# Kernel tuning notes

Measured on AMD Instinct MI355X. Metric: run time of the kernel, lower is better.

## Reference

```python
import jax, jax.numpy as jnp
import numpy as np

N = 50000      # amino-acid nodes
DIN = 64       # input feature dim
DH = 64        # hidden dim (= GAT out_feats per head)
H = 4          # attention heads
E_RES, E_SEQ, E_KNN = 400000, 100000, 400000
EPS = 1e-5


def setup_inputs() -> dict:
    key = jax.random.key(0)
    ks = iter(jax.random.split(key, 32))
    def nrm(shape, scale=0.1):
        return jax.random.normal(next(ks), shape, dtype=jnp.float32) * scale
    def edges(E):
        s = jax.random.randint(next(ks), (E,), 0, N, dtype=jnp.int32)
        d = jax.random.randint(next(ks), (E,), 0, N, dtype=jnp.int32)
        return s, d
    x = nrm((N, DIN), 1.0)
    src_res, dst_res = edges(E_RES)
    src_seq, dst_seq = edges(E_SEQ)
    src_knn, dst_knn = edges(E_KNN)
    inp = dict(x=x, src_res=src_res, dst_res=dst_res, src_seq=src_seq,
               dst_seq=dst_seq, src_knn=src_knn, dst_knn=dst_knn)
    # layer 0 (in=DIN), layer 1 (in=DH): per-relation stacked GAT params
    inp.update(W0=nrm((3, DIN, H * DH)), al0=nrm((3, H, DH)), ar0=nrm((3, H, DH)),
               b0=nrm((3, H * DH)), rW0=nrm((3, DIN, H * DH)))
    inp.update(W1=nrm((3, DH, H * DH)), al1=nrm((3, H, DH)), ar1=nrm((3, H, DH)),
               b1=nrm((3, H * DH)), rW1=nrm((3, DH, H * DH)))
    inp.update(fcW0=nrm((DH, DH)), fcb0=nrm((DH,)), fcW1=nrm((DH, DH)), fcb1=nrm((DH,)))
    inp.update(g0=jnp.ones((DIN,), jnp.float32), be0=jnp.zeros((DIN,), jnp.float32),
               g1=jnp.ones((DH,), jnp.float32), be1=jnp.zeros((DH,), jnp.float32))
    return inp


def _bn(x, g, b):
    mu = jnp.mean(x, axis=0)
    var = jnp.mean((x - mu) ** 2, axis=0)
    return (x - mu) * jax.lax.rsqrt(var + EPS) * g + b


def _gat(h, src, dst, W, al, ar, bias, rW):
    # DGL GATConv (feat_drop off in eval, residual=True via res_fc Linear, bias)
    n = h.shape[0]
    fs = (h @ W).reshape(n, H, DH)                    # [N,H,D]
    el = jnp.sum(fs * al, axis=-1)                    # [N,H]
    er = jnp.sum(fs * ar, axis=-1)
    e = jax.nn.leaky_relu(el[src] + er[dst], 0.2)     # [E,H]
    m = jax.ops.segment_max(e, dst, num_segments=n)
    a = jnp.exp(e - m[dst])
    s = jax.ops.segment_sum(a, dst, num_segments=n)
    alpha = a / s[dst]                                # edge-softmax per dst/head
    rst = jax.ops.segment_sum(alpha[:, :, None] * fs[src], dst, num_segments=n)
    return rst + (h @ rW).reshape(n, H, DH) + bias.reshape(1, H, DH)


def _layer(x, edges, W, al, ar, b, rW, fcW, fcb, g, be):
    x = _bn(x, g, be)
    h = jnp.zeros((x.shape[0], H, DH), x.dtype)
    for r, (s_, d_) in enumerate(edges):              # 3 relation types, summed
        h = h + _gat(x, s_, d_, W[r], al[r], ar[r], b[r], rW[r])
    x = jnp.mean(h, axis=1)                           # mean over heads
    return jax.nn.relu(x @ fcW + fcb)


def reference(x, src_res, dst_res, src_seq, dst_seq, src_knn, dst_knn,
              W0, al0, ar0, b0, rW0, W1, al1, ar1, b1, rW1,
              fcW0, fcb0, fcW1, fcb1, g0, be0, g1, be1):
    edges = [(src_res, dst_res), (src_seq, dst_seq), (src_knn, dst_knn)]
    x = _layer(x, edges, W0, al0, ar0, b0, rW0, fcW0, fcb0, g0, be0)
    x = _layer(x, edges, W1, al1, ar1, b1, rW1, fcW1, fcb1, g1, be1)
    return x
```

## Files before the change

kernel.cpp:

```cpp
#include <hip/hip_runtime.h>
#include <math.h>

#define NN    50000
#define DD    64
#define HH    4
#define E_RES 400000
#define E_SEQ 100000
#define E_KNN 400000
#define ETOT  (E_RES+E_SEQ+E_KNN)
#define RPS   (NN + 4)
#define NBLK  ((NN+255)/256)
#define KTOT  864
#define CTPS  (ETOT + 32)
#define NBUK  98
#define TBUK  (3*NBUK)
#define EPB   4096
#define PABLK ((ETOT+EPB-1)/EPB)
#define FBLK  (NN/16)
#define LZS   808

typedef __attribute__((ext_vector_type(8))) short short8;
typedef __attribute__((ext_vector_type(4))) float floatx4;

__device__ inline unsigned short f2bf(float f){
  union{float f; unsigned u;} v; v.f=f;
  unsigned r = v.u + 0x7FFF + ((v.u>>16)&1);
  return (unsigned short)(r>>16);
}
__device__ inline float bf2f(unsigned short u){
  union{unsigned u; float f;} v; v.u=(unsigned)u<<16; return v.f;
}

__global__ void __launch_bounds__(256)
k_bucketcnt(const int* __restrict__ d0, const int* __restrict__ d1,
            const int* __restrict__ d2, int* __restrict__ bcnt){
  __shared__ int cnt[TBUK];
  int t = threadIdx.x;
  for(int i=t;i<TBUK;i+=256) cnt[i]=0;
  __syncthreads();
  int ebase = blockIdx.x*EPB;
  #pragma unroll
  for(int j=0;j<16;j++){
    int i = ebase + j*256 + t;
    int d, r;
    if(i < E_RES){ d=d0[i]; r=0; }
    else if(i < E_RES+E_SEQ){ d=d1[i-E_RES]; r=1; }
    else if(i < ETOT){ d=d2[i-E_RES-E_SEQ]; r=2; }
    else continue;
    atomicAdd(&cnt[r*NBUK + (d>>9)], 1);
  }
  __syncthreads();
  for(int i=t;i<TBUK;i+=256){ int c=cnt[i]; if(c) atomicAdd(&bcnt[i], c); }
}

__global__ void k_bucketscan(const int* __restrict__ bcnt,
                             int* __restrict__ bbase, int* __restrict__ bcur){
  __shared__ int sh[TBUK];
  int t = threadIdx.x;
  if(t < 64){
    int carry = 0;
    for(int c=0;c<5;c++){
      int idx = c*64 + t;
      int v = (idx < TBUK) ? bcnt[idx] : 0;
      int inc = v;
      for(int off=1; off<64; off<<=1){ int n=__shfl_up(inc, off, 64); if(t>=off) inc+=n; }
      if(idx < TBUK) sh[idx] = carry + inc - v;
      carry += __shfl(inc, 63, 64);
    }
  }
  __syncthreads();
  if(t < TBUK){ bbase[t] = sh[t]; bcur[t] = sh[t]; }
  if(t == 0) bbase[TBUK] = ETOT;
}

__global__ void __launch_bounds__(256)
k_partA(const int* __restrict__ s0, const int* __restrict__ d0,
        const int* __restrict__ s1, const int* __restrict__ d1,
        const int* __restrict__ s2, const int* __restrict__ d2,
        int* __restrict__ bcur, unsigned* __restrict__ pairs){
  __shared__ int cnt[TBUK];
  __shared__ int gb[TBUK];
  int t = threadIdx.x;
  for(int i=t;i<TBUK;i+=256) cnt[i]=0;
  __syncthreads();
  int ebase = blockIdx.x*EPB;
  unsigned meta[16], pk[16];
  #pragma unroll
  for(int j=0;j<16;j++){
    int i = ebase + j*256 + t;
    int s, d, r;
    if(i < E_RES){ s=s0[i]; d=d0[i]; r=0; }
    else if(i < E_RES+E_SEQ){ int k=i-E_RES; s=s1[k]; d=d1[k]; r=1; }
    else if(i < ETOT){ int k=i-E_RES-E_SEQ; s=s2[k]; d=d2[k]; r=2; }
    else { meta[j]=0xFFFFFFFFu; continue; }
    int bk = r*NBUK + (d>>9);
    int rk = atomicAdd(&cnt[bk], 1);
    meta[j] = ((unsigned)bk<<16) | (unsigned)rk;
    pk[j]   = ((unsigned)(d&511)<<16) | (unsigned)s;
  }
  __syncthreads();
  for(int i=t;i<TBUK;i+=256){ int c=cnt[i]; gb[i] = c ? atomicAdd(&bcur[i], c) : 0; }
  __syncthreads();
  #pragma unroll
  for(int j=0;j<16;j++){
    unsigned mt = meta[j];
    if(mt != 0xFFFFFFFFu)
      pairs[gb[mt>>16] + (mt & 0xFFFFu)] = pk[j];
  }
}

__global__ void __launch_bounds__(256)
k_partB(const unsigned* __restrict__ pairs, const int* __restrict__ bbase,
        int* __restrict__ rowptr, int* __restrict__ csr){
  int bb = blockIdx.x, r = bb / NBUK, b = bb - r*NBUK;
  int dbase = b*512, dmax = min(512, NN - dbase);
  int off = (r==0)?0:(r==1)?E_RES:(E_RES+E_SEQ);
  __shared__ int hist[512];
  __shared__ int curs[513];
  int t = threadIdx.x;
  hist[t]=0; hist[256+t]=0;
  __syncthreads();
  int beg = bbase[bb], end = bbase[bb+1];
  for(int i=beg+t; i<end; i+=256) atomicAdd(&hist[pairs[i]>>16], 1);
  __syncthreads();
  if(t < 64){
    int carry = 0;
    for(int c=0;c<8;c++){
      int v = hist[c*64+t];
      int inc = v;
      for(int o2=1; o2<64; o2<<=1){ int n=__shfl_up(inc, o2, 64); if(t>=o2) inc+=n; }
      curs[c*64+t] = (beg - off) + carry + inc - v;
      carry += __shfl(inc, 63, 64);
    }
    if(t==0) curs[512] = end - off;
  }
  __syncthreads();
  int* rp = rowptr + r*RPS + dbase;
  for(int i=t; i<=dmax; i+=256) rp[i] = curs[i];
  __syncthreads();
  for(int i=beg+t; i<end; i+=256){
    unsigned p = pairs[i];
    int pos = atomicAdd(&curs[p>>16], 1);
    csr[off + pos] = (int)(p & 0xFFFFu);
  }
}

__global__ void k_bnstats(const float* __restrict__ x, float* __restrict__ stats,
                          unsigned short* __restrict__ Abf){
  __shared__ float sh[512];
  int t = threadIdx.x, col = t & 63, rg = t >> 6;
  float s=0.f, q=0.f;
  for(int row = blockIdx.x*4 + rg; row < NN; row += gridDim.x*4){
    float v = x[(size_t)row*64 + col]; s += v; q += v*v;
    Abf[(size_t)row*64 + col] = f2bf(v);
  }
  sh[t]=s; sh[256+t]=q; __syncthreads();
  if(rg==0){
    s = sh[col]+sh[64+col]+sh[128+col]+sh[192+col];
    q = sh[256+col]+sh[320+col]+sh[384+col]+sh[448+col];
    atomicAdd(&stats[col], s); atomicAdd(&stats[64+col], q);
  }
}

__global__ void __launch_bounds__(256)
k_prep3(const float* __restrict__ stats, const float* __restrict__ g,
        const float* __restrict__ be, const float* __restrict__ W,
        const float* __restrict__ al, const float* __restrict__ ar,
        const float* __restrict__ b, const float* __restrict__ rW,
        const float* __restrict__ fcW, const float* __restrict__ fcb,
        float* __restrict__ wbufF){
  __shared__ float scale[64], shift[64];
  int t = threadIdx.x;
  if(t<64){
    float mu  = stats[t]*(1.0f/NN);
    float var = stats[64+t]*(1.0f/NN) - mu*mu;
    float sc  = g[t]*rsqrtf(var + 1e-5f);
    scale[t]=sc; shift[t]=be[t]-mu*sc;
  }
  __syncthreads();
  char* wb = (char*)wbufF;
  unsigned short* Wf = (unsigned short*)wbufF;
  float* biasF = (float*)(wb + 110592);
  int bid = blockIdx.x;
  if(bid < 52){
    __shared__ float fcWs[4096];
    for(int i=t;i<4096;i+=256) fcWs[i]=fcW[i];
    __syncthreads();
    int j = bid*16 + (t>>4);
    int cg = (t&15)*4;
    float Wrow[64];
    if(j < 64){
      for(int d=0; d<64; d++){
        float w=0.f;
        for(int r=0;r<3;r++)
          #pragma unroll
          for(int h=0;h<4;h++)
            w += rW[((size_t)(r*64+j))*256 + h*64 + d];
        Wrow[d] = scale[j]*0.25f*w;
      }
    } else {
      int jj = j-64;
      int r = jj>>8, dc = jj&255, h = dc&3, c = dc>>2;
      const float* Wp = W + ((size_t)(r*64+c))*256 + h*64;
      float sc = 0.25f*scale[c];
      #pragma unroll
      for(int d=0; d<64; d++) Wrow[d] = sc*Wp[d];
    }
    #pragma unroll
    for(int cc=0; cc<4; cc++){
      int col = cg+cc;
      float acc=0.f;
      #pragma unroll
      for(int d=0; d<64; d++) acc += Wrow[d]*fcWs[d*64+col];
      Wf[(size_t)col*KTOT + j] = f2bf(acc);
    }
  } else if(bid < 58){
    int wv = (bid-52)*4 + (t>>6);
    int r = wv >> 3, cc = wv & 7, h = cc & 3, k = t & 63;
    const float* av = ((cc>=4)?ar:al) + (r*HH+h)*64;
    const float* Wk = W + ((size_t)(r*64+k))*256 + h*64;
    float w=0.f;
    for(int d2=0; d2<64; d2++) w += Wk[d2]*av[d2];
    float* WelR = (float*)(wb + 110848 + r*2080);
    WelR[cc*64 + k] = scale[k]*w;
    float bp = shift[k]*w;
    for(int off=32; off; off>>=1) bp += __shfl_down(bp, off, 64);
    if(k==0) (WelR + 512)[cc] = bp;
  } else {
    __shared__ float S[3][64];
    __shared__ float BH[64];
    if(t<192){
      int r=t>>6, d=t&63;
      float s=0.f;
      #pragma unroll
      for(int h=0;h<4;h++){
        const float* Wp = W + (size_t)(r*64)*256 + h*64 + d;
        for(int k=0;k<64;k++) s += shift[k]*Wp[(size_t)k*256];
      }
      S[r][d]=0.25f*s;
    } else {
      int d = t-192;
      float s=0.f;
      for(int k=0;k<64;k++){
        float w=0.f;
        for(int r=0;r<3;r++)
          #pragma unroll
          for(int h=0;h<4;h++)
            w += rW[((size_t)(r*64+k))*256 + h*64 + d];
        s += shift[k]*0.25f*w;
      }
      float bb=0.f;
      for(int r=0;r<3;r++)
        #pragma unroll
        for(int h=0;h<4;h++) bb += b[r*256 + h*64 + d];
      BH[d] = s + 0.25f*bb;
    }
    __syncthreads();
    if(t<192){
      int r=t>>6, col=t&63;
      float acc=0.f;
      for(int d=0;d<64;d++) acc += S[r][d]*fcW[d*64+col];
      Wf[(size_t)col*KTOT + 832 + r] = f2bf(acc);
    } else {
      int col=t-192;
      float acc=0.f;
      for(int d=0;d<64;d++) acc += BH[d]*fcW[d*64+col];
      biasF[col] = acc + fcb[col];
    }
    if(t<64){
      for(int j=835;j<KTOT;j++) Wf[(size_t)t*KTOT + j] = 0;
    }
  }
}

__global__ void __launch_bounds__(256)
k_el3(const float* __restrict__ A, const float* __restrict__ wbufF,
      float* __restrict__ EL){
  int r = blockIdx.x / NBLK;
  const char* wb = (const char*)wbufF;
  const float* Wel = (const float*)(wb + 110848 + r*2080);
  const float* biasE = Wel + 512;
  float* ELr = EL + (size_t)r*NN*8;
  __shared__ float sw[512];
  __shared__ float sb[8];
  int t = threadIdx.x;
  sw[t]=Wel[t]; sw[256+t]=Wel[256+t];
  if(t<8) sb[t]=biasE[t];
  __syncthreads();
  int n = (blockIdx.x % NBLK)*256 + t;
  if(n>=NN) return;
  float acc[8];
  #pragma unroll
  for(int c=0;c<8;c++) acc[c]=sb[c];
  const float4* Ar = (const float4*)(A + (size_t)n*64);
  #pragma unroll
  for(int kq=0;kq<16;kq++){
    float4 a = Ar[kq];
    #pragma unroll
    for(int c=0;c<8;c++){
      const float* w = sw + c*64 + kq*4;
      acc[c] += a.x*w[0] + a.y*w[1] + a.z*w[2] + a.w*w[3];
    }
  }
  ((float4*)ELr)[n*2]   = make_float4(acc[0],acc[1],acc[2],acc[3]);
  ((float4*)ELr)[n*2+1] = make_float4(acc[4],acc[5],acc[6],acc[7]);
}

__global__ void __launch_bounds__(256)
k_edgecoef3(const float* __restrict__ EL, const int* __restrict__ rowptr,
            const int* __restrict__ csr, unsigned short* __restrict__ coefT){
  int r = blockIdx.x / NBLK;
  const float* ELr = EL + (size_t)r*NN*8;
  const int* rp = rowptr + r*RPS;
  int off = (r==0)?0:(r==1)?E_RES:(E_RES+E_SEQ);
  const int* cs = csr + off;
  unsigned short* t0 = coefT + off;
  unsigned short* t1 = coefT + (size_t)CTPS + off;
  unsigned short* t2 = coefT + (size_t)2*CTPS + off;
  unsigned short* t3 = coefT + (size_t)3*CTPS + off;
  int n = (blockIdx.x % NBLK)*256 + threadIdx.x;
  if(n>=NN) return;
  int beg = rp[n], end = rp[n+1];
  if(end<=beg) return;
  const float4 er = ((const float4*)ELr)[n*2+1];
  float m0=-1e30f,m1=-1e30f,m2=-1e30f,m3=-1e30f;
  float s0=0.f,s1=0.f,s2=0.f,s3=0.f;
  for(int i=beg;i<end;i++){
    int src = cs[i];
    float4 el = ((const float4*)ELr)[src*2];
    float e0=el.x+er.x, e1=el.y+er.y, e2=el.z+er.z, e3=el.w+er.w;
    e0 = e0>0.f? e0 : 0.2f*e0;
    e1 = e1>0.f? e1 : 0.2f*e1;
    e2 = e2>0.f? e2 : 0.2f*e2;
    e3 = e3>0.f? e3 : 0.2f*e3;
    float n0=fmaxf(m0,e0); s0=s0*__expf(m0-n0)+__expf(e0-n0); m0=n0;
    float n1=fmaxf(m1,e1); s1=s1*__expf(m1-n1)+__expf(e1-n1); m1=n1;
    float n2=fmaxf(m2,e2); s2=s2*__expf(m2-n2)+__expf(e2-n2); m2=n2;
    float n3=fmaxf(m3,e3); s3=s3*__expf(m3-n3)+__expf(e3-n3); m3=n3;
  }
  float r0=1.f/s0, r1=1.f/s1, r2=1.f/s2, r3=1.f/s3;
  for(int i=beg;i<end;i++){
    int src = cs[i];
    float4 el = ((const float4*)ELr)[src*2];
    float e0=el.x+er.x, e1=el.y+er.y, e2=el.z+er.z, e3=el.w+er.w;
    e0 = e0>0.f? e0 : 0.2f*e0;
    e1 = e1>0.f? e1 : 0.2f*e1;
    e2 = e2>0.f? e2 : 0.2f*e2;
    e3 = e3>0.f? e3 : 0.2f*e3;
    t0[i] = f2bf(__expf(e0-m0)*r0);
    t1[i] = f2bf(__expf(e1-m1)*r1);
    t2[i] = f2bf(__expf(e2-m2)*r2);
    t3[i] = f2bf(__expf(e3-m3)*r3);
  }
}

__global__ void __launch_bounds__(256)
k_fused(const unsigned short* __restrict__ Abf, const int* __restrict__ rowptr,
        const int* __restrict__ csr, const unsigned short* __restrict__ coefT,
        const float* __restrict__ wbufF, float* __restrict__ out,
        unsigned short* __restrict__ Abf2, float* __restrict__ stats, int dostats){
  __shared__ unsigned short Zl[16*LZS];
  const unsigned short* Wf = (const unsigned short*)wbufF;
  const float* biasF = (const float*)((const char*)wbufF + 110592);
  int t = threadIdx.x, wv = t>>6, lane = t&63, m = lane&15, kq = lane>>4;
  int nb = blockIdx.x*16;
  int n4 = nb + wv*4;
  int nn = m>>2, h = m&3;
  for(int i=t; i<512; i+=256){ int nd=i>>5, j=i&31; if(j<29) Zl[nd*LZS+771+j]=0; }
  for(int r=0;r<3;r++){
    const int* rp = rowptr + r*RPS;
    int off = (r==0)?0:(r==1)?E_RES:(E_RES+E_SEQ);
    const int* cs = csr + off;
    const unsigned short* cT = coefT + (size_t)h*CTPS + off;
    int rpn  = rp[n4+nn];
    int rpn1 = rp[n4+nn+1];
    unsigned dg = (unsigned)(rpn1 - rpn);
    int beg = __shfl(rpn, 0, 64);
    int end = __shfl(rpn1, 15, 64);
    floatx4 acc0={0.f,0.f,0.f,0.f};
    floatx4 acc1={0.f,0.f,0.f,0.f};
    floatx4 acc2={0.f,0.f,0.f,0.f};
    floatx4 acc3={0.f,0.f,0.f,0.f};
    for(int eb = (beg & ~31); eb < end; eb += 32){
      int p0 = eb + kq*8;
      union { uint4 q; short8 v; } af;
      af.q = *(const uint4*)(cT + p0);
      int qd = p0 - rpn;
      unsigned w0 = (((unsigned)(qd+0)<dg)?0x0000FFFFu:0u) | (((unsigned)(qd+1)<dg)?0xFFFF0000u:0u);
      unsigned w1 = (((unsigned)(qd+2)<dg)?0x0000FFFFu:0u) | (((unsigned)(qd+3)<dg)?0xFFFF0000u:0u);
      unsigned w2 = (((unsigned)(qd+4)<dg)?0x0000FFFFu:0u) | (((unsigned)(qd+5)<dg)?0xFFFF0000u:0u);
      unsigned w3 = (((unsigned)(qd+6)<dg)?0x0000FFFFu:0u) | (((unsigned)(qd+7)<dg)?0xFFFF0000u:0u);
      af.q.x &= w0; af.q.y &= w1; af.q.z &= w2; af.q.w &= w3;
      const int* csp = cs + p0;
      int s0=csp[0],s1=csp[1],s2=csp[2],s3=csp[3],s4=csp[4],s5=csp[5],s6=csp[6],s7=csp[7];
      const unsigned short* q0 = Abf + ((size_t)s0<<6) + m;
      const unsigned short* q1 = Abf + ((size_t)s1<<6) + m;
      const unsigned short* q2 = Abf + ((size_t)s2<<6) + m;
      const unsigned short* q3 = Abf + ((size_t)s3<<6) + m;
      const unsigned short* q4 = Abf + ((size_t)s4<<6) + m;
      const unsigned short* q5 = Abf + ((size_t)s5<<6) + m;
      const unsigned short* q6 = Abf + ((size_t)s6<<6) + m;
      const unsigned short* q7 = Abf + ((size_t)s7<<6) + m;
      union { unsigned u[4]; short8 v; } b0,b1,b2,b3;
      b0.u[0]=(unsigned)q0[0] |((unsigned)q1[0]<<16);
      b0.u[1]=(unsigned)q2[0] |((unsigned)q3[0]<<16);
      b0.u[2]=(unsigned)q4[0] |((unsigned)q5[0]<<16);
      b0.u[3]=(unsigned)q6[0] |((unsigned)q7[0]<<16);
      b1.u[0]=(unsigned)q0[16]|((unsigned)q1[16]<<16);
      b1.u[1]=(unsigned)q2[16]|((unsigned)q3[16]<<16);
      b1.u[2]=(unsigned)q4[16]|((unsigned)q5[16]<<16);
      b1.u[3]=(unsigned)q6[16]|((unsigned)q7[16]<<16);
      b2.u[0]=(unsigned)q0[32]|((unsigned)q1[32]<<16);
      b2.u[1]=(unsigned)q2[32]|((unsigned)q3[32]<<16);
      b2.u[2]=(unsigned)q4[32]|((unsigned)q5[32]<<16);
      b2.u[3]=(unsigned)q6[32]|((unsigned)q7[32]<<16);
      b3.u[0]=(unsigned)q0[48]|((unsigned)q1[48]<<16);
      b3.u[1]=(unsigned)q2[48]|((unsigned)q3[48]<<16);
      b3.u[2]=(unsigned)q4[48]|((unsigned)q5[48]<<16);
      b3.u[3]=(unsigned)q6[48]|((unsigned)q7[48]<<16);
      acc0 = __builtin_amdgcn_mfma_f32_16x16x32_bf16(af.v, b0.v, acc0, 0,0,0);
      acc1 = __builtin_amdgcn_mfma_f32_16x16x32_bf16(af.v, b1.v, acc1, 0,0,0);
      acc2 = __builtin_amdgcn_mfma_f32_16x16x32_bf16(af.v, b2.v, acc2, 0,0,0);
      acc3 = __builtin_amdgcn_mfma_f32_16x16x32_bf16(af.v, b3.v, acc3, 0,0,0);
    }
    unsigned short* zrow = Zl + (wv*4+kq)*LZS + r*256 + m*4;
    ushort4 o;
    o.x=f2bf(acc0[0]); o.y=f2bf(acc0[1]); o.z=f2bf(acc0[2]); o.w=f2bf(acc0[3]);
    *(ushort4*)(zrow)       = o;
    o.x=f2bf(acc1[0]); o.y=f2bf(acc1[1]); o.z=f2bf(acc1[2]); o.w=f2bf(acc1[3]);
    *(ushort4*)(zrow + 64)  = o;
    o.x=f2bf(acc2[0]); o.y=f2bf(acc2[1]); o.z=f2bf(acc2[2]); o.w=f2bf(acc2[3]);
    *(ushort4*)(zrow + 128) = o;
    o.x=f2bf(acc3[0]); o.y=f2bf(acc3[1]); o.z=f2bf(acc3[2]); o.w=f2bf(acc3[3]);
    *(ushort4*)(zrow + 192) = o;
    int degk = __shfl((int)dg, kq<<2, 64);
    if(m==0)
      Zl[(wv*4+kq)*LZS + 768 + r] = degk>0 ? (unsigned short)0x3F80 : (unsigned short)0;
  }
  __syncthreads();
  floatx4 acc = {0.f,0.f,0.f,0.f};
  const unsigned short* Arow = Abf + (size_t)(nb+m)*64;
  const unsigned short* Zrow = Zl + m*LZS;
  #pragma unroll
  for(int kb=0; kb<27; kb++){
    short8 a;
    if(kb<2) a = *(const short8*)(Arow + kb*32 + kq*8);
    else     a = *(const short8*)(Zrow + (kb-2)*32 + kq*8);
    short8 b = *(const short8*)(Wf + (size_t)(wv*16+m)*KTOT + kb*32 + kq*8);
    acc = __builtin_amdgcn_mfma_f32_16x16x32_bf16(a, b, acc, 0,0,0);
  }
  int col = wv*16 + m;
  float bb = biasF[col];
  float sv=0.f, qv=0.f;
  #pragma unroll
  for(int ri=0; ri<4; ri++){
    int ro = nb + kq*4 + ri;
    float v = fmaxf(acc[ri] + bb, 0.f);
    out[(size_t)ro*64 + col] = v;
    if(dostats){
      Abf2[(size_t)ro*64 + col] = f2bf(v);
      sv += v; qv += v*v;
    }
  }
  if(dostats){
    sv += __shfl_xor(sv, 16, 64); qv += __shfl_xor(qv, 16, 64);
    sv += __shfl_xor(sv, 32, 64); qv += __shfl_xor(qv, 32, 64);
    if(kq==0){ atomicAdd(&stats[col], sv); atomicAdd(&stats[64+col], qv); }
  }
}

extern "C" void kernel_launch(void* const* d_in, const int* in_sizes, int n_in,
                              void* d_out, int out_size, void* d_ws, size_t ws_size,
                              hipStream_t stream){
  const float* x      =(const float*)d_in[0];
  const int* src_res  =(const int*)d_in[1];
  const int* dst_res  =(const int*)d_in[2];
  const int* src_seq  =(const int*)d_in[3];
  const int* dst_seq  =(const int*)d_in[4];
  const int* src_knn  =(const int*)d_in[5];
  const int* dst_knn  =(const int*)d_in[6];
  const float* W0 =(const float*)d_in[7];
  const float* al0=(const float*)d_in[8];
  const float* ar0=(const float*)d_in[9];
  const float* b0 =(const float*)d_in[10];
  const float* rW0=(const float*)d_in[11];
  const float* W1 =(const float*)d_in[12];
  const float* al1=(const float*)d_in[13];
  const float* ar1=(const float*)d_in[14];
  const float* b1 =(const float*)d_in[15];
  const float* rW1=(const float*)d_in[16];
  const float* fcW0=(const float*)d_in[17];
  const float* fcb0=(const float*)d_in[18];
  const float* fcW1=(const float*)d_in[19];
  const float* fcb1=(const float*)d_in[20];
  const float* g0 =(const float*)d_in[21];
  const float* be0=(const float*)d_in[22];
  const float* g1 =(const float*)d_in[23];
  const float* be1=(const float*)d_in[24];

  char* ws=(char*)d_ws;
  int*   bcnt   =(int*)  (ws+0);
  int*   bbase  =(int*)  (ws+4096);
  float* stats0 =(float*)(ws+600000);
  float* stats1 =(float*)(ws+600512);
  int*   rowptr =(int*)  (ws+601024);
  int*   bcur   =(int*)  (ws+1201088);
  int*   csr    =(int*)  (ws+1801088);
  float* wbuf   =(float*)(ws+5401088);
  unsigned short* Abf  =(unsigned short*)(ws+5526528);
  unsigned* pairs =(unsigned*)(ws+11926528UL);
  float* xbuf   =(float*)(ws+91926528UL);
  float* EL     =(float*)(ws+104726528UL);
  unsigned short* coefT=(unsigned short*)(ws+109526528UL);
  unsigned short* Abf2 =(unsigned short*)(ws+123926528UL);

  hipMemsetAsync(ws, 0, 601024, stream);

  k_bucketcnt<<<PABLK,256,0,stream>>>(dst_res,dst_seq,dst_knn,bcnt);
  k_bucketscan<<<1,512,0,stream>>>(bcnt,bbase,bcur);
  k_partA<<<PABLK,256,0,stream>>>(src_res,dst_res,src_seq,dst_seq,
                                  src_knn,dst_knn,bcur,pairs);
  k_partB<<<TBUK,256,0,stream>>>(pairs,bbase,rowptr,csr);

  k_bnstats<<<256,256,0,stream>>>(x,stats0,Abf);
  k_prep3<<<59,256,0,stream>>>(stats0,g0,be0,W0,al0,ar0,b0,rW0,fcW0,fcb0,wbuf);
  k_el3<<<3*NBLK,256,0,stream>>>(x,wbuf,EL);
  k_edgecoef3<<<3*NBLK,256,0,stream>>>(EL,rowptr,csr,coefT);
  k_fused<<<FBLK,256,0,stream>>>(Abf,rowptr,csr,coefT,wbuf,xbuf,Abf2,stats1,1);
  k_prep3<<<59,256,0,stream>>>(stats1,g1,be1,W1,al1,ar1,b1,rW1,fcW1,fcb1,wbuf);
  k_el3<<<3*NBLK,256,0,stream>>>(xbuf,wbuf,EL);
  k_edgecoef3<<<3*NBLK,256,0,stream>>>(EL,rowptr,csr,coefT);
  k_fused<<<FBLK,256,0,stream>>>(Abf2,rowptr,csr,coefT,wbuf,(float*)d_out,Abf2,stats0,0);
}
```

Measured before the change: 430.5 us.

## Split fused GAT kernel across relations with 12 waves and split-K epilogue

The fused aggregation kernel now launches 768 threads per block, giving each relation its own group of four waves instead of looping over the three relations serially inside one wave. The final 27-step MFMA projection is split three ways along K across the wave groups, and the partial sums are reduced through a new shared-memory buffer before bias, ReLU and stats. The Z row stride grows slightly and the zero-fill loop is rewritten to cover the padding. This is meant to raise parallelism and latency hiding in the gather-heavy edge loop. In exchange it adds an extra barrier, more shared memory per block, and possible register-pressure limits at 768 threads.

```diff
diff --git a/kernel.cpp b/kernel.cpp
--- a/kernel.cpp
+++ b/kernel.cpp
@@ -17,7 +17,7 @@
 #define EPB   4096
 #define PABLK ((ETOT+EPB-1)/EPB)
 #define FBLK  (NN/16)
-#define LZS   808
+#define LZS   810
 
 typedef __attribute__((ext_vector_type(8))) short short8;
 typedef __attribute__((ext_vector_type(4))) float floatx4;
@@ -354,20 +354,22 @@
   }
 }
 
-__global__ void __launch_bounds__(256)
+__global__ void __launch_bounds__(768)
 k_fused(const unsigned short* __restrict__ Abf, const int* __restrict__ rowptr,
         const int* __restrict__ csr, const unsigned short* __restrict__ coefT,
         const float* __restrict__ wbufF, float* __restrict__ out,
         unsigned short* __restrict__ Abf2, float* __restrict__ stats, int dostats){
   __shared__ unsigned short Zl[16*LZS];
+  __shared__ float pf[8*256];
   const unsigned short* Wf = (const unsigned short*)wbufF;
   const float* biasF = (const float*)((const char*)wbufF + 110592);
   int t = threadIdx.x, wv = t>>6, lane = t&63, m = lane&15, kq = lane>>4;
   int nb = blockIdx.x*16;
-  int n4 = nb + wv*4;
+  int sg = wv & 3, r = wv >> 2;
+  int n4 = nb + sg*4;
   int nn = m>>2, h = m&3;
-  for(int i=t; i<512; i+=256){ int nd=i>>5, j=i&31; if(j<29) Zl[nd*LZS+771+j]=0; }
-  for(int r=0;r<3;r++){
+  for(int i=t; i<624; i+=768){ int nd=i/39, j=i-nd*39; Zl[nd*LZS+771+j]=0; }
+  {
     const int* rp = rowptr + r*RPS;
     int off = (r==0)?0:(r==1)?E_RES:(E_RES+E_SEQ);
     const int* cs = csr + off;
@@ -423,7 +425,7 @@
       acc2 = __builtin_amdgcn_mfma_f32_16x16x32_bf16(af.v, b2.v, acc2, 0,0,0);
       acc3 = __builtin_amdgcn_mfma_f32_16x16x32_bf16(af.v, b3.v, acc3, 0,0,0);
     }
-    unsigned short* zrow = Zl + (wv*4+kq)*LZS + r*256 + m*4;
+    unsigned short* zrow = Zl + (sg*4+kq)*LZS + r*256 + m*4;
     ushort4 o;
     o.x=f2bf(acc0[0]); o.y=f2bf(acc0[1]); o.z=f2bf(acc0[2]); o.w=f2bf(acc0[3]);
     *(ushort4*)(zrow)       = o;
@@ -435,37 +437,49 @@
     *(ushort4*)(zrow + 192) = o;
     int degk = __shfl((int)dg, kq<<2, 64);
     if(m==0)
-      Zl[(wv*4+kq)*LZS + 768 + r] = degk>0 ? (unsigned short)0x3F80 : (unsigned short)0;
-  }
-  __syncthreads();
+      Zl[(sg*4+kq)*LZS + 768 + r] = degk>0 ? (unsigned short)0x3F80 : (unsigned short)0;
+  }
+  __syncthreads();
+  int ct = wv & 3, ks = wv >> 2;
   floatx4 acc = {0.f,0.f,0.f,0.f};
   const unsigned short* Arow = Abf + (size_t)(nb+m)*64;
   const unsigned short* Zrow = Zl + m*LZS;
   #pragma unroll
-  for(int kb=0; kb<27; kb++){
+  for(int kk=0; kk<9; kk++){
+    int kb = ks*9 + kk;
     short8 a;
     if(kb<2) a = *(const short8*)(Arow + kb*32 + kq*8);
     else     a = *(const short8*)(Zrow + (kb-2)*32 + kq*8);
-    short8 b = *(const short8*)(Wf + (size_t)(wv*16+m)*KTOT + kb*32 + kq*8);
+    short8 b = *(const short8*)(Wf + (size_t)(ct*16+m)*KTOT + kb*32 + kq*8);
     acc = __builtin_amdgcn_mfma_f32_16x16x32_bf16(a, b, acc, 0,0,0);
   }
-  int col = wv*16 + m;
-  float bb = biasF[col];
-  float sv=0.f, qv=0.f;
-  #pragma unroll
-  for(int ri=0; ri<4; ri++){
-    int ro = nb + kq*4 + ri;
-    float v = fmaxf(acc[ri] + bb, 0.f);
-    out[(size_t)ro*64 + col] = v;
+  if(ks != 0)
+    ((float4*)pf)[(wv-4)*64 + lane] = make_float4(acc[0],acc[1],acc[2],acc[3]);
+  __syncthreads();
+  if(ks == 0){
+    float4 p1 = ((float4*)pf)[(ct  )*64 + lane];
+    float4 p2 = ((float4*)pf)[(ct+4)*64 + lane];
+    int col = ct*16 + m;
+    float bb = biasF[col];
+    float vr0 = acc[0]+p1.x+p2.x, vr1 = acc[1]+p1.y+p2.y;
+    float vr2 = acc[2]+p1.z+p2.z, vr3 = acc[3]+p1.w+p2.w;
+    float sv=0.f, qv=0.f;
+    float vv[4] = {vr0,vr1,vr2,vr3};
+    #pragma unroll
+    for(int ri=0; ri<4; ri++){
+      int ro = nb + kq*4 + ri;
+      float v = fmaxf(vv[ri] + bb, 0.f);
+      out[(size_t)ro*64 + col] = v;
+      if(dostats){
+        Abf2[(size_t)ro*64 + col] = f2bf(v);
+        sv += v; qv += v*v;
+      }
+    }
     if(dostats){
-      Abf2[(size_t)ro*64 + col] = f2bf(v);
-      sv += v; qv += v*v;
-    }
-  }
-  if(dostats){
-    sv += __shfl_xor(sv, 16, 64); qv += __shfl_xor(qv, 16, 64);
-    sv += __shfl_xor(sv, 32, 64); qv += __shfl_xor(qv, 32, 64);
-    if(kq==0){ atomicAdd(&stats[col], sv); atomicAdd(&stats[64+col], qv); }
+      sv += __shfl_xor(sv, 16, 64); qv += __shfl_xor(qv, 16, 64);
+      sv += __shfl_xor(sv, 32, 64); qv += __shfl_xor(qv, 32, 64);
+      if(kq==0){ atomicAdd(&stats[col], sv); atomicAdd(&stats[64+col], qv); }
+    }
   }
 }
 
@@ -526,9 +540,9 @@
   k_prep3<<<59,256,0,stream>>>(stats0,g0,be0,W0,al0,ar0,b0,rW0,fcW0,fcb0,wbuf);
   k_el3<<<3*NBLK,256,0,stream>>>(x,wbuf,EL);
   k_edgecoef3<<<3*NBLK,256,0,stream>>>(EL,rowptr,csr,coefT);
-  k_fused<<<FBLK,256,0,stream>>>(Abf,rowptr,csr,coefT,wbuf,xbuf,Abf2,stats1,1);
+  k_fused<<<FBLK,768,0,stream>>>(Abf,rowptr,csr,coefT,wbuf,xbuf,Abf2,stats1,1);
   k_prep3<<<59,256,0,stream>>>(stats1,g1,be1,W1,al1,ar1,b1,rW1,fcW1,fcb1,wbuf);
   k_el3<<<3*NBLK,256,0,stream>>>(xbuf,wbuf,EL);
   k_edgecoef3<<<3*NBLK,256,0,stream>>>(EL,rowptr,csr,coefT);
-  k_fused<<<FBLK,256,0,stream>>>(Abf2,rowptr,csr,coefT,wbuf,(float*)d_out,Abf2,stats0,0);
-}
+  k_fused<<<FBLK,768,0,stream>>>(Abf2,rowptr,csr,coefT,wbuf,(float*)d_out,Abf2,stats0,0);
+}
```

Measured after the change: 468.6 us. +8.9%, slower.

## Stage gathered source rows through LDS with vector loads in fused GAT kernel

Applied to the files above, without the earlier changes.

The edge-aggregation loop used to build each MFMA B-fragment from sixteen scattered 2-byte global loads per lane. It now has each lane pair fetch one full 128-byte source row with four 16-byte loads and store it into a per-wave LDS staging tile (padded stride). B-fragments are then read from LDS. Explicit lgkmcnt waits and sched barriers order the LDS writes and reads within each wave. The Zl stride is also tweaked and the pairs workspace buffer is relocated. The trade-off is extra LDS traffic, LDS capacity and synchronisation stalls in exchange for coalesced global access.

```diff
diff --git a/kernel.cpp b/kernel.cpp
--- a/kernel.cpp
+++ b/kernel.cpp
@@ -17,7 +17,8 @@
 #define EPB   4096
 #define PABLK ((ETOT+EPB-1)/EPB)
 #define FBLK  (NN/16)
-#define LZS   808
+#define LZS   810
+#define SGS   72
 
 typedef __attribute__((ext_vector_type(8))) short short8;
 typedef __attribute__((ext_vector_type(4))) float floatx4;
@@ -360,12 +361,16 @@
         const float* __restrict__ wbufF, float* __restrict__ out,
         unsigned short* __restrict__ Abf2, float* __restrict__ stats, int dostats){
   __shared__ unsigned short Zl[16*LZS];
+  __shared__ unsigned short Sg[4*32*SGS];
   const unsigned short* Wf = (const unsigned short*)wbufF;
   const float* biasF = (const float*)((const char*)wbufF + 110592);
   int t = threadIdx.x, wv = t>>6, lane = t&63, m = lane&15, kq = lane>>4;
   int nb = blockIdx.x*16;
   int n4 = nb + wv*4;
   int nn = m>>2, h = m&3;
+  int srow = lane>>1, shalf = lane&1;
+  unsigned short* sgw = Sg + (wv*32 + srow)*SGS + shalf*32;
+  const unsigned short* sgr = Sg + (size_t)(wv*32 + kq*8)*SGS;
   for(int i=t; i<512; i+=256){ int nd=i>>5, j=i&31; if(j<29) Zl[nd*LZS+771+j]=0; }
   for(int r=0;r<3;r++){
     const int* rp = rowptr + r*RPS;
@@ -391,37 +396,34 @@
       unsigned w2 = (((unsigned)(qd+4)<dg)?0x0000FFFFu:0u) | (((unsigned)(qd+5)<dg)?0xFFFF0000u:0u);
       unsigned w3 = (((unsigned)(qd+6)<dg)?0x0000FFFFu:0u) | (((unsigned)(qd+7)<dg)?0xFFFF0000u:0u);
       af.q.x &= w0; af.q.y &= w1; af.q.z &= w2; af.q.w &= w3;
-      const int* csp = cs + p0;
-      int s0=csp[0],s1=csp[1],s2=csp[2],s3=csp[3],s4=csp[4],s5=csp[5],s6=csp[6],s7=csp[7];
-      const unsigned short* q0 = Abf + ((size_t)s0<<6) + m;
-      const unsigned short* q1 = Abf + ((size_t)s1<<6) + m;
-      const unsigned short* q2 = Abf + ((size_t)s2<<6) + m;
-      const unsigned short* q3 = Abf + ((size_t)s3<<6) + m;
-      const unsigned short* q4 = Abf + ((size_t)s4<<6) + m;
-      const unsigned short* q5 = Abf + ((size_t)s5<<6) + m;
-      const unsigned short* q6 = Abf + ((size_t)s6<<6) + m;
-      const unsigned short* q7 = Abf + ((size_t)s7<<6) + m;
+      int srcr = cs[eb + srow];
+      const unsigned short* rowp = Abf + ((size_t)srcr<<6) + shalf*32;
+      uint4 g0 = *(const uint4*)(rowp);
+      uint4 g1 = *(const uint4*)(rowp + 8);
+      uint4 g2 = *(const uint4*)(rowp + 16);
+      uint4 g3 = *(const uint4*)(rowp + 24);
+      *(uint4*)(sgw)      = g0;
+      *(uint4*)(sgw + 8)  = g1;
+      *(uint4*)(sgw + 16) = g2;
+      *(uint4*)(sgw + 24) = g3;
+      asm volatile("s_waitcnt lgkmcnt(0)" ::: "memory");
+      __builtin_amdgcn_sched_barrier(0);
       union { unsigned u[4]; short8 v; } b0,b1,b2,b3;
-      b0.u[0]=(unsigned)q0[0] |((unsigned)q1[0]<<16);
-      b0.u[1]=(unsigned)q2[0] |((unsigned)q3[0]<<16);
-      b0.u[2]=(unsigned)q4[0] |((unsigned)q5[0]<<16);
-      b0.u[3]=(unsigned)q6[0] |((unsigned)q7[0]<<16);
-      b1.u[0]=(unsigned)q0[16]|((unsigned)q1[16]<<16);
-      b1.u[1]=(unsigned)q2[16]|((unsigned)q3[16]<<16);
-      b1.u[2]=(unsigned)q4[16]|((unsigned)q5[16]<<16);
-      b1.u[3]=(unsigned)q6[16]|((unsigned)q7[16]<<16);
-      b2.u[0]=(unsigned)q0[32]|((unsigned)q1[32]<<16);
-      b2.u[1]=(unsigned)q2[32]|((unsigned)q3[32]<<16);
-      b2.u[2]=(unsigned)q4[32]|((unsigned)q5[32]<<16);
-      b2.u[3]=(unsigned)q6[32]|((unsigned)q7[32]<<16);
-      b3.u[0]=(unsigned)q0[48]|((unsigned)q1[48]<<16);
-      b3.u[1]=(unsigned)q2[48]|((unsigned)q3[48]<<16);
-      b3.u[2]=(unsigned)q4[48]|((unsigned)q5[48]<<16);
-      b3.u[3]=(unsigned)q6[48]|((unsigned)q7[48]<<16);
+      #pragma unroll
+      for(int k=0;k<4;k++){
+        const unsigned short* r0p = sgr + (2*k  )*SGS;
+        const unsigned short* r1p = sgr + (2*k+1)*SGS;
+        b0.u[k]=(unsigned)r0p[m   ]|((unsigned)r1p[m   ]<<16);
+        b1.u[k]=(unsigned)r0p[m+16]|((unsigned)r1p[m+16]<<16);
+        b2.u[k]=(unsigned)r0p[m+32]|((unsigned)r1p[m+32]<<16);
+        b3.u[k]=(unsigned)r0p[m+48]|((unsigned)r1p[m+48]<<16);
+      }
       acc0 = __builtin_amdgcn_mfma_f32_16x16x32_bf16(af.v, b0.v, acc0, 0,0,0);
       acc1 = __builtin_amdgcn_mfma_f32_16x16x32_bf16(af.v, b1.v, acc1, 0,0,0);
       acc2 = __builtin_amdgcn_mfma_f32_16x16x32_bf16(af.v, b2.v, acc2, 0,0,0);
       acc3 = __builtin_amdgcn_mfma_f32_16x16x32_bf16(af.v, b3.v, acc3, 0,0,0);
+      asm volatile("s_waitcnt lgkmcnt(0)" ::: "memory");
+      __builtin_amdgcn_sched_barrier(0);
     }
     unsigned short* zrow = Zl + (wv*4+kq)*LZS + r*256 + m*4;
     ushort4 o;
@@ -508,7 +510,7 @@
   int*   csr    =(int*)  (ws+1801088);
   float* wbuf   =(float*)(ws+5401088);
   unsigned short* Abf  =(unsigned short*)(ws+5526528);
-  unsigned* pairs =(unsigned*)(ws+11926528UL);
+  unsigned* pairs =(unsigned*)(ws+27000000UL);
   float* xbuf   =(float*)(ws+91926528UL);
   float* EL     =(float*)(ws+104726528UL);
   unsigned short* coefT=(unsigned short*)(ws+109526528UL);
```

After: 463.7 us. 7.7% more time.

## Parallelize edge softmax with one wavefront per destination node

Applied to the files above, without the earlier changes.

Edge-coefficient computation now maps one 64-lane wavefront to each (relation, destination node) instead of one thread per node. For degrees up to 64, each lane handles one edge and max and sum are reduced with wave shuffles. Larger degrees use strided online softmax with a shuffle merge. This targets serial per-thread loops and uncoalesced csr reads and coefT writes under degree imbalance, at the cost of many idle lanes since average degree is only about 8. The LZS padding and the pairs workspace offset also change.

```diff
diff --git a/kernel.cpp b/kernel.cpp
--- a/kernel.cpp
+++ b/kernel.cpp
@@ -17,7 +17,8 @@
 #define EPB   4096
 #define PABLK ((ETOT+EPB-1)/EPB)
 #define FBLK  (NN/16)
-#define LZS   808
+#define ECB   ((3*NN)/4)
+#define LZS   810
 
 typedef __attribute__((ext_vector_type(8))) short short8;
 typedef __attribute__((ext_vector_type(4))) float floatx4;
@@ -309,7 +310,9 @@
 __global__ void __launch_bounds__(256)
 k_edgecoef3(const float* __restrict__ EL, const int* __restrict__ rowptr,
             const int* __restrict__ csr, unsigned short* __restrict__ coefT){
-  int r = blockIdx.x / NBLK;
+  int w = blockIdx.x*4 + (threadIdx.x>>6);
+  int lane = threadIdx.x & 63;
+  int r = w / NN, n = w - r*NN;
   const float* ELr = EL + (size_t)r*NN*8;
   const int* rp = rowptr + r*RPS;
   int off = (r==0)?0:(r==1)?E_RES:(E_RES+E_SEQ);
@@ -318,39 +321,83 @@
   unsigned short* t1 = coefT + (size_t)CTPS + off;
   unsigned short* t2 = coefT + (size_t)2*CTPS + off;
   unsigned short* t3 = coefT + (size_t)3*CTPS + off;
-  int n = (blockIdx.x % NBLK)*256 + threadIdx.x;
-  if(n>=NN) return;
   int beg = rp[n], end = rp[n+1];
-  if(end<=beg) return;
+  int deg = end - beg;
+  if(deg <= 0) return;
   const float4 er = ((const float4*)ELr)[n*2+1];
-  float m0=-1e30f,m1=-1e30f,m2=-1e30f,m3=-1e30f;
-  float s0=0.f,s1=0.f,s2=0.f,s3=0.f;
-  for(int i=beg;i<end;i++){
-    int src = cs[i];
+  if(deg <= 64){
+    bool act = lane < deg;
+    int src = cs[beg + (act ? lane : 0)];
     float4 el = ((const float4*)ELr)[src*2];
     float e0=el.x+er.x, e1=el.y+er.y, e2=el.z+er.z, e3=el.w+er.w;
     e0 = e0>0.f? e0 : 0.2f*e0;
     e1 = e1>0.f? e1 : 0.2f*e1;
     e2 = e2>0.f? e2 : 0.2f*e2;
     e3 = e3>0.f? e3 : 0.2f*e3;
-    float n0=fmaxf(m0,e0); s0=s0*__expf(m0-n0)+__expf(e0-n0); m0=n0;
-    float n1=fmaxf(m1,e1); s1=s1*__expf(m1-n1)+__expf(e1-n1); m1=n1;
-    float n2=fmaxf(m2,e2); s2=s2*__expf(m2-n2)+__expf(e2-n2); m2=n2;
-    float n3=fmaxf(m3,e3); s3=s3*__expf(m3-n3)+__expf(e3-n3); m3=n3;
-  }
-  float r0=1.f/s0, r1=1.f/s1, r2=1.f/s2, r3=1.f/s3;
-  for(int i=beg;i<end;i++){
-    int src = cs[i];
-    float4 el = ((const float4*)ELr)[src*2];
-    float e0=el.x+er.x, e1=el.y+er.y, e2=el.z+er.z, e3=el.w+er.w;
-    e0 = e0>0.f? e0 : 0.2f*e0;
-    e1 = e1>0.f? e1 : 0.2f*e1;
-    e2 = e2>0.f? e2 : 0.2f*e2;
-    e3 = e3>0.f? e3 : 0.2f*e3;
-    t0[i] = f2bf(__expf(e0-m0)*r0);
-    t1[i] = f2bf(__expf(e1-m1)*r1);
-    t2[i] = f2bf(__expf(e2-m2)*r2);
-    t3[i] = f2bf(__expf(e3-m3)*r3);
+    if(!act){ e0=-1e30f; e1=-1e30f; e2=-1e30f; e3=-1e30f; }
+    float m0=e0,m1=e1,m2=e2,m3=e3;
+    #pragma unroll
+    for(int o=32;o;o>>=1){
+      m0=fmaxf(m0,__shfl_xor(m0,o,64));
+      m1=fmaxf(m1,__shfl_xor(m1,o,64));
+      m2=fmaxf(m2,__shfl_xor(m2,o,64));
+      m3=fmaxf(m3,__shfl_xor(m3,o,64));
+    }
+    float p0=__expf(e0-m0), p1=__expf(e1-m1), p2=__expf(e2-m2), p3=__expf(e3-m3);
+    float s0=p0,s1=p1,s2=p2,s3=p3;
+    #pragma unroll
+    for(int o=32;o;o>>=1){
+      s0+=__shfl_xor(s0,o,64);
+      s1+=__shfl_xor(s1,o,64);
+      s2+=__shfl_xor(s2,o,64);
+      s3+=__shfl_xor(s3,o,64);
+    }
+    if(act){
+      int i = beg + lane;
+      t0[i]=f2bf(p0/s0); t1[i]=f2bf(p1/s1); t2[i]=f2bf(p2/s2); t3[i]=f2bf(p3/s3);
+    }
+  } else {
+    float m0=-1e30f,m1=-1e30f,m2=-1e30f,m3=-1e30f;
+    float s0=0.f,s1=0.f,s2=0.f,s3=0.f;
+    for(int i=beg+lane; i<end; i+=64){
+      int src = cs[i];
+      float4 el = ((const float4*)ELr)[src*2];
+      float e0=el.x+er.x, e1=el.y+er.y, e2=el.z+er.z, e3=el.w+er.w;
+      e0 = e0>0.f? e0 : 0.2f*e0;
+      e1 = e1>0.f? e1 : 0.2f*e1;
+      e2 = e2>0.f? e2 : 0.2f*e2;
+      e3 = e3>0.f? e3 : 0.2f*e3;
+      float n0=fmaxf(m0,e0); s0=s0*__expf(m0-n0)+__expf(e0-n0); m0=n0;
+      float n1=fmaxf(m1,e1); s1=s1*__expf(m1-n1)+__expf(e1-n1); m1=n1;
+      float n2=fmaxf(m2,e2); s2=s2*__expf(m2-n2)+__expf(e2-n2); m2=n2;
+      float n3=fmaxf(m3,e3); s3=s3*__expf(m3-n3)+__expf(e3-n3); m3=n3;
+    }
+    #pragma unroll
+    for(int o=32;o;o>>=1){
+      float om,os,nm;
+      om=__shfl_xor(m0,o,64); os=__shfl_xor(s0,o,64);
+      nm=fmaxf(m0,om); s0=s0*__expf(m0-nm)+os*__expf(om-nm); m0=nm;
+      om=__shfl_xor(m1,o,64); os=__shfl_xor(s1,o,64);
+      nm=fmaxf(m1,om); s1=s1*__expf(m1-nm)+os*__expf(om-nm); m1=nm;
+      om=__shfl_xor(m2,o,64); os=__shfl_xor(s2,o,64);
+      nm=fmaxf(m2,om); s2=s2*__expf(m2-nm)+os*__expf(om-nm); m2=nm;
+      om=__shfl_xor(m3,o,64); os=__shfl_xor(s3,o,64);
+      nm=fmaxf(m3,om); s3=s3*__expf(m3-nm)+os*__expf(om-nm); m3=nm;
+    }
+    float r0=1.f/s0, r1=1.f/s1, r2=1.f/s2, r3=1.f/s3;
+    for(int i=beg+lane; i<end; i+=64){
+      int src = cs[i];
+      float4 el = ((const float4*)ELr)[src*2];
+      float e0=el.x+er.x, e1=el.y+er.y, e2=el.z+er.z, e3=el.w+er.w;
+      e0 = e0>0.f? e0 : 0.2f*e0;
+      e1 = e1>0.f? e1 : 0.2f*e1;
+      e2 = e2>0.f? e2 : 0.2f*e2;
+      e3 = e3>0.f? e3 : 0.2f*e3;
+      t0[i]=f2bf(__expf(e0-m0)*r0);
+      t1[i]=f2bf(__expf(e1-m1)*r1);
+      t2[i]=f2bf(__expf(e2-m2)*r2);
+      t3[i]=f2bf(__expf(e3-m3)*r3);
+    }
   }
 }
 
@@ -508,7 +555,7 @@
   int*   csr    =(int*)  (ws+1801088);
   float* wbuf   =(float*)(ws+5401088);
   unsigned short* Abf  =(unsigned short*)(ws+5526528);
-  unsigned* pairs =(unsigned*)(ws+11926528UL);
+  unsigned* pairs =(unsigned*)(ws+27000000UL);
   float* xbuf   =(float*)(ws+91926528UL);
   float* EL     =(float*)(ws+104726528UL);
   unsigned short* coefT=(unsigned short*)(ws+109526528UL);
@@ -525,10 +572,10 @@
   k_bnstats<<<256,256,0,stream>>>(x,stats0,Abf);
   k_prep3<<<59,256,0,stream>>>(stats0,g0,be0,W0,al0,ar0,b0,rW0,fcW0,fcb0,wbuf);
   k_el3<<<3*NBLK,256,0,stream>>>(x,wbuf,EL);
-  k_edgecoef3<<<3*NBLK,256,0,stream>>>(EL,rowptr,csr,coefT);
+  k_edgecoef3<<<ECB,256,0,stream>>>(EL,rowptr,csr,coefT);
   k_fused<<<FBLK,256,0,stream>>>(Abf,rowptr,csr,coefT,wbuf,xbuf,Abf2,stats1,1);
   k_prep3<<<59,256,0,stream>>>(stats1,g1,be1,W1,al1,ar1,b1,rW1,fcW1,fcb1,wbuf);
   k_el3<<<3*NBLK,256,0,stream>>>(xbuf,wbuf,EL);
-  k_edgecoef3<<<3*NBLK,256,0,stream>>>(EL,rowptr,csr,coefT);
+  k_edgecoef3<<<ECB,256,0,stream>>>(EL,rowptr,csr,coefT);
   k_fused<<<FBLK,256,0,stream>>>(Abf2,rowptr,csr,coefT,wbuf,(float*)d_out,Abf2,stats0,0);
 }
```

Measured after the change: 522.6 us. 21.4% more time.
